# Optimization experiments

Hardware: AMD Instinct MI355X
Metric: run time of the kernel (lower is better)

The kernel has to match this reference:

```python
import jax, jax.numpy as jnp
import numpy as np
import math

N_QUBITS = 8
N_QLAYERS = 1
LN_EPS = 1e-5


def _rx(state, theta, wire, n):
    # state: (N, 2,...,2) complex64 with n qubit axes; theta: (N,)
    sh = (theta.shape[0],) + (1,) * (n - 1)
    c = jnp.cos(theta / 2).reshape(sh)
    s = jnp.sin(theta / 2).reshape(sh)
    a = jax.lax.index_in_dim(state, 0, wire + 1, keepdims=False)
    b = jax.lax.index_in_dim(state, 1, wire + 1, keepdims=False)
    return jnp.stack([c * a - 1j * s * b, -1j * s * a + c * b], axis=wire + 1)


def _cnot(state, cw, tw, n):
    s0 = jax.lax.index_in_dim(state, 0, cw + 1, keepdims=False)
    s1 = jax.lax.index_in_dim(state, 1, cw + 1, keepdims=False)
    t_ax = tw + 1 if tw < cw else tw  # target axis index after removing control axis
    s1 = jnp.flip(s1, axis=t_ax)
    return jnp.stack([s0, s1], axis=cw + 1)


def _quantum(angles, qweights):
    # AngleEmbedding (RX) + BasicEntanglerLayers (RX + CNOT ring) + PauliZ expvals
    # angles: (N, 8) float; qweights: (1, 8) float -> returns (N, 8) float
    n = N_QUBITS
    N = angles.shape[0]
    state = jnp.zeros((N,) + (2,) * n, jnp.complex64)
    state = state.at[(slice(None),) + (0,) * n].set(1.0 + 0j)
    for w in range(n):
        state = _rx(state, angles[:, w], w, n)
    for l in range(N_QLAYERS):
        for w in range(n):
            state = _rx(state, jnp.broadcast_to(qweights[l, w], (N,)), w, n)
        for cw in range(n):
            state = _cnot(state, cw, (cw + 1) % n, n)
    probs = state.real ** 2 + state.imag ** 2
    zs = []
    for w in range(n):
        p = probs.sum(axis=tuple(a for a in range(1, n + 1) if a != w + 1))  # (N, 2)
        zs.append(p[:, 0] - p[:, 1])
    return jnp.stack(zs, axis=-1)


def _layernorm(x, g, b):
    m = x.mean(-1, keepdims=True)
    v = ((x - m) ** 2).mean(-1, keepdims=True)
    return (x - m) / jnp.sqrt(v + LN_EPS) * g + b


def _forward(x, Wq, Wk, Wv, Wo, ln1_g, ln1_b, W1, b1, W2, b2, ln2_g, ln2_b,
             ql1_w, ql1_b, qweights, ql2_w, ql2_b):
    B, S, D = x.shape
    H = 16
    dk = D // H
    q = (x @ Wq.T).reshape(B, S, H, dk)
    k = (x @ Wk.T).reshape(B, S, H, dk)
    v = (x @ Wv.T).reshape(B, S, H, dk)
    scores = jnp.einsum('bqhd,bkhd->bhqk', q, k) * (1.0 / math.sqrt(dk))
    attn = jax.nn.softmax(scores, axis=-1)
    o = jnp.einsum('bhqk,bkhd->bqhd', attn, v).reshape(B, S, D) @ Wo.T
    x = _layernorm(o + x, ln1_g, ln1_b)
    ff = jax.nn.relu(x @ W1.T + b1) @ W2.T + b2
    x = _layernorm(ff + x, ln2_g, ln2_b)
    angles = (x @ ql1_w.T + ql1_b).reshape(B * S, N_QUBITS)
    z = _quantum(angles, qweights).reshape(B, S, N_QUBITS).astype(x.dtype)
    y = jnp.concatenate([z, x], axis=2) @ ql2_w.T + ql2_b
    return y


def setup_inputs() -> dict:
    key = jax.random.key(0)
    ks = jax.random.split(key, 12)
    B, S, D, F = 4, 1024, 1024, 4096
    sc = 0.02
    w = lambda k, *sh: jax.random.normal(k, sh, jnp.float32) * sc
    return {
        'x': jax.random.normal(ks[0], (B, S, D), jnp.float32),
        'Wq': w(ks[1], D, D), 'Wk': w(ks[2], D, D), 'Wv': w(ks[3], D, D), 'Wo': w(ks[4], D, D),
        'ln1_g': jnp.ones((D,), jnp.float32), 'ln1_b': jnp.zeros((D,), jnp.float32),
        'W1': w(ks[5], F, D), 'b1': jnp.zeros((F,), jnp.float32),
        'W2': w(ks[6], D, F), 'b2': jnp.zeros((D,), jnp.float32),
        'ln2_g': jnp.ones((D,), jnp.float32), 'ln2_b': jnp.zeros((D,), jnp.float32),
        'ql1_w': w(ks[7], N_QUBITS, D), 'ql1_b': jnp.zeros((N_QUBITS,), jnp.float32),
        'qweights': jax.random.uniform(ks[8], (N_QLAYERS, N_QUBITS), jnp.float32, 0.0, 2 * np.pi),
        'ql2_w': w(ks[9], D, D + N_QUBITS), 'ql2_b': jnp.zeros((D,), jnp.float32),
    }


def reference(x, Wq, Wk, Wv, Wo, ln1_g, ln1_b, W1, b1, W2, b2, ln2_g, ln2_b,
              ql1_w, ql1_b, qweights, ql2_w, ql2_b):
    return _forward(x, Wq, Wk, Wv, Wo, ln1_g, ln1_b, W1, b1, W2, b2, ln2_g, ln2_b,
                    ql1_w, ql1_b, qweights, ql2_w, ql2_b)
```

## Files before the change

### kernel.cpp

```cpp
#include <hip/hip_runtime.h>
#include <hip/hip_bf16.h>

typedef __bf16 bf16_t;
typedef __attribute__((ext_vector_type(8))) __bf16 bf16x8;
typedef __attribute__((ext_vector_type(4))) float floatx4;

#define BM 128

enum { EPI_NONE = 0, EPI_RESID, EPI_BIAS_RELU, EPI_BIAS_RESID, EPI_QL2 };

__device__ __forceinline__ void gld_lds16(const bf16_t* g, bf16_t* l) {
  __builtin_amdgcn_global_load_lds(
      (__attribute__((address_space(1))) void*)(g),
      (__attribute__((address_space(3))) void*)(l), 16, 0, 0);
}

template<int ROWS, int COLS>
__device__ __forceinline__ void stage_swz(const bf16_t* g, int ld, bf16_t* lds, int tid) {
  constexpr int G = COLS / 8;
  #pragma unroll
  for (int i = 0; i < ROWS * G / 256; ++i) {
    int ci = i * 256 + tid;
    int row = ci / G, cc = ci % G;
    int gg = (G == 8) ? (cc ^ (row & 7)) : ((cc & 8) | ((cc & 7) ^ (row & 7)));
    gld_lds16(g + (size_t)row * ld + gg * 8, lds + ci * 8);
  }
}

__device__ __forceinline__ void core128(const bf16_t* __restrict__ Ag,
                                        const bf16_t* __restrict__ Bg,
                                        int K, int ldb,
                                        bf16_t* As, bf16_t* Bs,
                                        floatx4 acc[4][4]) {
  const int tid = threadIdx.x;
  const int wid = tid >> 6, lane = tid & 63;
  const int wm = (wid >> 1) * 64, wn = (wid & 1) * 64;
  const int m16 = lane & 15, quad = lane >> 4;
  const int r7 = m16 & 7;
  for (int k0 = 0; k0 < K; k0 += 64) {
    stage_swz<128, 64>(Ag + k0, K, As, tid);
    stage_swz<128, 64>(Bg + k0, ldb, Bs, tid);
    __syncthreads();
    #pragma unroll
    for (int ks = 0; ks < 2; ++ks) {
      const int gi = ks * 4 + quad;
      const int slot = gi ^ r7;
      bf16x8 af[4], bfr[4];
      #pragma unroll
      for (int mt = 0; mt < 4; ++mt)
        af[mt] = *(const bf16x8*)&As[((wm + mt * 16 + m16) * 8 + slot) * 8];
      #pragma unroll
      for (int nt = 0; nt < 4; ++nt)
        bfr[nt] = *(const bf16x8*)&Bs[((wn + nt * 16 + m16) * 8 + slot) * 8];
      #pragma unroll
      for (int mt = 0; mt < 4; ++mt)
        #pragma unroll
        for (int nt = 0; nt < 4; ++nt)
          acc[mt][nt] = __builtin_amdgcn_mfma_f32_16x16x32_bf16(af[mt], bfr[nt], acc[mt][nt], 0, 0, 0);
    }
    __syncthreads();
  }
}

template<int EPI>
__global__ __launch_bounds__(256)
void gemm128(const bf16_t* __restrict__ A, const bf16_t* __restrict__ B,
             bf16_t* __restrict__ C, const float* __restrict__ bias,
             int N, int K) {
  __shared__ bf16_t As[BM * 64];
  __shared__ bf16_t Bs[BM * 64];
  const int tid = threadIdx.x;
  const int wid = tid >> 6, lane = tid & 63;
  const int wm = (wid >> 1) * 64, wn = (wid & 1) * 64;
  const int m16 = lane & 15, quad = lane >> 4;
  const int m0 = blockIdx.y * BM, n0 = blockIdx.x * BM;
  floatx4 acc[4][4];
  const floatx4 vzero = {0.f, 0.f, 0.f, 0.f};
  #pragma unroll
  for (int mt = 0; mt < 4; ++mt)
    #pragma unroll
    for (int nt = 0; nt < 4; ++nt) acc[mt][nt] = vzero;
  core128(A + (size_t)m0 * K, B + (size_t)n0 * K, K, K, As, Bs, acc);
  #pragma unroll
  for (int mt = 0; mt < 4; ++mt)
    #pragma unroll
    for (int nt = 0; nt < 4; ++nt) {
      const int gcol = n0 + wn + nt * 16 + m16;
      float bv = (EPI == EPI_BIAS_RELU) ? bias[gcol] : 0.f;
      #pragma unroll
      for (int r = 0; r < 4; ++r) {
        const int grow = m0 + wm + mt * 16 + quad * 4 + r;
        float v = acc[mt][nt][r];
        if (EPI == EPI_BIAS_RELU) { v += bv; v = fmaxf(v, 0.f); }
        C[(size_t)grow * N + gcol] = (bf16_t)v;
      }
    }
}

__global__ __launch_bounds__(256)
void gemm_qkv(const bf16_t* __restrict__ X, const bf16_t* __restrict__ Wb,
              bf16_t* __restrict__ Qo, bf16_t* __restrict__ Ko, bf16_t* __restrict__ Vt) {
  __shared__ bf16_t As[BM * 64];
  __shared__ bf16_t Bs[BM * 64];
  const int tid = threadIdx.x;
  const int wid = tid >> 6, lane = tid & 63;
  const int wm = (wid >> 1) * 64, wn = (wid & 1) * 64;
  const int m16 = lane & 15, quad = lane >> 4;
  const int m0 = blockIdx.y * BM, n0 = blockIdx.x * BM;
  const int sel = blockIdx.z;
  const bf16_t* B = Wb + (size_t)sel * 1024 * 1024;
  floatx4 acc[4][4];
  const floatx4 vzero = {0.f, 0.f, 0.f, 0.f};
  #pragma unroll
  for (int mt = 0; mt < 4; ++mt)
    #pragma unroll
    for (int nt = 0; nt < 4; ++nt) acc[mt][nt] = vzero;
  core128(X + (size_t)m0 * 1024, B + (size_t)n0 * 1024, 1024, 1024, As, Bs, acc);
  if (sel < 2) {
    bf16_t* C = sel ? Ko : Qo;
    const float sc = sel ? 1.f : 0.125f;
    #pragma unroll
    for (int mt = 0; mt < 4; ++mt)
      #pragma unroll
      for (int nt = 0; nt < 4; ++nt) {
        const int gcol = n0 + wn + nt * 16 + m16;
        #pragma unroll
        for (int r = 0; r < 4; ++r) {
          const int grow = m0 + wm + mt * 16 + quad * 4 + r;
          C[(size_t)grow * 1024 + gcol] = (bf16_t)(acc[mt][nt][r] * sc);
        }
      }
  } else {
    #pragma unroll
    for (int mt = 0; mt < 4; ++mt) {
      const int grow0 = m0 + wm + mt * 16 + quad * 4;
      const int b = grow0 >> 10, s = grow0 & 1023;
      #pragma unroll
      for (int nt = 0; nt < 4; ++nt) {
        const int gcol = n0 + wn + nt * 16 + m16;
        const int h = gcol >> 6, d = gcol & 63;
        #pragma unroll
        for (int r = 0; r < 4; ++r)
          Vt[(((size_t)b * 16 + h) * 64 + d) * 1024 + s + r] = (bf16_t)acc[mt][nt][r];
      }
    }
  }
}

template<int EPI, bool OUTF32>
__global__ __launch_bounds__(256)
void gemm64(const bf16_t* __restrict__ A, const bf16_t* __restrict__ B,
            void* __restrict__ Cv,
            const bf16_t* __restrict__ resid, const float* __restrict__ bias,
            const bf16_t* __restrict__ z, const float* __restrict__ zw,
            int N, int K, int ldb, int boff, int mblocks) {
  __shared__ bf16_t As[BM * 128];
  __shared__ bf16_t Bs[64 * 128];
  const int tid = threadIdx.x;
  const int wid = tid >> 6, lane = tid & 63;
  const int wm = (wid >> 1) * 64, wn = (wid & 1) * 32;
  const int m16 = lane & 15, quad = lane >> 4;
  const int r7 = m16 & 7;
  const int id = blockIdx.x;
  const int m0 = (id % mblocks) * BM, n0 = (id / mblocks) * 64;
  const bf16_t* Ag = A + (size_t)m0 * K;
  const bf16_t* Bg = B + (size_t)n0 * ldb + boff;
  floatx4 acc[4][2];
  const floatx4 vzero = {0.f, 0.f, 0.f, 0.f};
  #pragma unroll
  for (int mt = 0; mt < 4; ++mt)
    #pragma unroll
    for (int nt = 0; nt < 2; ++nt) acc[mt][nt] = vzero;
  for (int k0 = 0; k0 < K; k0 += 128) {
    stage_swz<128, 128>(Ag + k0, K, As, tid);
    stage_swz<64, 128>(Bg + k0, ldb, Bs, tid);
    __syncthreads();
    #pragma unroll
    for (int ks = 0; ks < 4; ++ks) {
      const int gi = ks * 4 + quad;
      const int slot = (gi & 8) | ((gi & 7) ^ r7);
      bf16x8 af[4], bfr[2];
      #pragma unroll
      for (int mt = 0; mt < 4; ++mt)
        af[mt] = *(const bf16x8*)&As[((wm + mt * 16 + m16) * 16 + slot) * 8];
      #pragma unroll
      for (int nt = 0; nt < 2; ++nt)
        bfr[nt] = *(const bf16x8*)&Bs[((wn + nt * 16 + m16) * 16 + slot) * 8];
      #pragma unroll
      for (int mt = 0; mt < 4; ++mt)
        #pragma unroll
        for (int nt = 0; nt < 2; ++nt)
          acc[mt][nt] = __builtin_amdgcn_mfma_f32_16x16x32_bf16(af[mt], bfr[nt], acc[mt][nt], 0, 0, 0);
    }
    __syncthreads();
  }
  #pragma unroll
  for (int mt = 0; mt < 4; ++mt)
    #pragma unroll
    for (int nt = 0; nt < 2; ++nt) {
      const int gcol = n0 + wn + nt * 16 + m16;
      float bv = 0.f;
      if (EPI == EPI_BIAS_RESID || EPI == EPI_QL2) bv = bias[gcol];
      #pragma unroll
      for (int r = 0; r < 4; ++r) {
        const int grow = m0 + wm + mt * 16 + quad * 4 + r;
        float v = acc[mt][nt][r];
        if (EPI == EPI_RESID) v += (float)resid[(size_t)grow * N + gcol];
        if (EPI == EPI_BIAS_RESID) v += bv + (float)resid[(size_t)grow * N + gcol];
        if (EPI == EPI_QL2) {
          float s = 0.f;
          #pragma unroll
          for (int u = 0; u < 8; ++u)
            s += (float)z[(size_t)grow * 8 + u] * zw[(size_t)gcol * 1032 + u];
          v += bv + s;
        }
        if (OUTF32) ((float*)Cv)[(size_t)grow * N + gcol] = v;
        else        ((bf16_t*)Cv)[(size_t)grow * N + gcol] = (bf16_t)v;
      }
    }
}

__global__ __launch_bounds__(256)
void attn_kernel(const bf16_t* __restrict__ Q, const bf16_t* __restrict__ Kb,
                 const bf16_t* __restrict__ Vt, bf16_t* __restrict__ O) {
  __shared__ bf16_t Qs[64 * 64];
  __shared__ bf16_t Ks[128 * 64];
  __shared__ bf16_t Vs[64 * 128];
  __shared__ bf16_t Ps[4][16 * 128];
  const int tid = threadIdx.x;
  const int wid = tid >> 6, lane = tid & 63;
  const int m16 = lane & 15, quad = lane >> 4;
  const int qt = blockIdx.x, bh = blockIdx.y;
  const int b = bh >> 4, h = bh & 15;
  const size_t qbase = ((size_t)(b * 1024 + qt * 64)) * 1024 + h * 64;
  #pragma unroll
  for (int i = 0; i < 2; ++i) {
    int ci = i * 256 + tid;
    int row = ci >> 3, cc = ci & 7;
    *(bf16x8*)&Qs[row * 64 + ((cc ^ (row & 7)) * 8)] =
        *(const bf16x8*)&Q[qbase + (size_t)row * 1024 + cc * 8];
  }
  __syncthreads();
  const int qm = wid * 16 + m16;
  bf16x8 qf0 = *(const bf16x8*)&Qs[qm * 64 + ((quad ^ (qm & 7)) * 8)];
  bf16x8 qf1 = *(const bf16x8*)&Qs[qm * 64 + (((4 + quad) ^ (qm & 7)) * 8)];
  floatx4 oacc[4];
  float rs[4];
  const floatx4 vzero = {0.f, 0.f, 0.f, 0.f};
  #pragma unroll
  for (int dt = 0; dt < 4; ++dt) oacc[dt] = vzero;
  #pragma unroll
  for (int r = 0; r < 4; ++r) rs[r] = 0.f;
  const size_t kbase = ((size_t)(b * 1024)) * 1024 + h * 64;
  const size_t vbase = ((size_t)bh * 64) * 1024;
  for (int kt = 0; kt < 8; ++kt) {
    __syncthreads();
    #pragma unroll
    for (int i = 0; i < 4; ++i) {
      int ci = i * 256 + tid;
      int row = ci >> 3, cc = ci & 7;
      *(bf16x8*)&Ks[row * 64 + ((cc ^ (row & 7)) * 8)] =
          *(const bf16x8*)&Kb[kbase + (size_t)(kt * 128 + row) * 1024 + cc * 8];
    }
    #pragma unroll
    for (int i = 0; i < 4; ++i) {
      int ci = i * 256 + tid;
      int dr = ci >> 4, cc = ci & 15;
      int gs = (cc & 8) | ((cc & 7) ^ (dr & 7));
      *(bf16x8*)&Vs[dr * 128 + gs * 8] =
          *(const bf16x8*)&Vt[vbase + (size_t)dr * 1024 + kt * 128 + cc * 8];
    }
    __syncthreads();
    floatx4 sa[8];
    #pragma unroll
    for (int nt = 0; nt < 8; ++nt) sa[nt] = vzero;
    #pragma unroll
    for (int nt = 0; nt < 8; ++nt) {
      const int n = nt * 16 + m16;
      bf16x8 kf0 = *(const bf16x8*)&Ks[n * 64 + ((quad ^ (n & 7)) * 8)];
      bf16x8 kf1 = *(const bf16x8*)&Ks[n * 64 + (((4 + quad) ^ (n & 7)) * 8)];
      sa[nt] = __builtin_amdgcn_mfma_f32_16x16x32_bf16(qf0, kf0, sa[nt], 0, 0, 0);
      sa[nt] = __builtin_amdgcn_mfma_f32_16x16x32_bf16(qf1, kf1, sa[nt], 0, 0, 0);
    }
    #pragma unroll
    for (int nt = 0; nt < 8; ++nt)
      #pragma unroll
      for (int r = 0; r < 4; ++r) {
        float pv = __expf(sa[nt][r]);
        rs[r] += pv;
        const int prow = quad * 4 + r;
        const int g = nt * 2 + (m16 >> 3);
        const int gs = (g & 8) | ((g & 7) ^ (prow & 7));
        Ps[wid][prow * 128 + gs * 8 + (m16 & 7)] = (bf16_t)pv;
      }
    bf16x8 pf[4];
    #pragma unroll
    for (int ksub = 0; ksub < 4; ++ksub) {
      const int g = ksub * 4 + quad;
      const int gs = (g & 8) | ((g & 7) ^ (m16 & 7));
      pf[ksub] = *(const bf16x8*)&Ps[wid][m16 * 128 + gs * 8];
    }
    #pragma unroll
    for (int dt = 0; dt < 4; ++dt) {
      const int n = dt * 16 + m16;
      #pragma unroll
      for (int ksub = 0; ksub < 4; ++ksub) {
        const int g = ksub * 4 + quad;
        const int gs = (g & 8) | ((g & 7) ^ (n & 7));
        bf16x8 vf = *(const bf16x8*)&Vs[n * 128 + gs * 8];
        oacc[dt] = __builtin_amdgcn_mfma_f32_16x16x32_bf16(pf[ksub], vf, oacc[dt], 0, 0, 0);
      }
    }
  }
  #pragma unroll
  for (int r = 0; r < 4; ++r) {
    rs[r] += __shfl_xor(rs[r], 1);
    rs[r] += __shfl_xor(rs[r], 2);
    rs[r] += __shfl_xor(rs[r], 4);
    rs[r] += __shfl_xor(rs[r], 8);
  }
  const size_t obase = ((size_t)(b * 1024 + qt * 64 + wid * 16)) * 1024 + h * 64;
  #pragma unroll
  for (int dt = 0; dt < 4; ++dt)
    #pragma unroll
    for (int r = 0; r < 4; ++r)
      O[obase + (size_t)(quad * 4 + r) * 1024 + dt * 16 + m16] = (bf16_t)(oacc[dt][r] / rs[r]);
}

struct Segs {
  const float* s[5];
  bf16_t* d[5];
  int n8[5];
};
__global__ __launch_bounds__(256)
void conv_multi(Segs sg) {
  const int zz = blockIdx.z;
  const float* in = sg.s[zz];
  bf16_t* out = sg.d[zz];
  const int n8 = sg.n8[zz];
  for (int i = blockIdx.x * 256 + threadIdx.x; i < n8; i += gridDim.x * 256) {
    const float* p = in + (size_t)i * 8;
    floatx4 a = *(const floatx4*)p;
    floatx4 b = *(const floatx4*)(p + 4);
    bf16x8 o;
    #pragma unroll
    for (int j = 0; j < 4; ++j) { o[j] = (bf16_t)a[j]; o[4 + j] = (bf16_t)b[j]; }
    *(bf16x8*)(out + (size_t)i * 8) = o;
  }
}

__global__ __launch_bounds__(256)
void ln_kernel(const bf16_t* __restrict__ in, const float* __restrict__ g,
               const float* __restrict__ b, bf16_t* __restrict__ out) {
  const int row = blockIdx.x * 4 + (threadIdx.x >> 6);
  const int lane = threadIdx.x & 63;
  const bf16_t* p = in + (size_t)row * 1024 + lane * 16;
  bf16x8 v0 = *(const bf16x8*)p;
  bf16x8 v1 = *(const bf16x8*)(p + 8);
  float f[16];
  #pragma unroll
  for (int j = 0; j < 8; ++j) { f[j] = (float)v0[j]; f[8 + j] = (float)v1[j]; }
  float s = 0.f, ss = 0.f;
  #pragma unroll
  for (int j = 0; j < 16; ++j) { s += f[j]; ss += f[j] * f[j]; }
  #pragma unroll
  for (int off = 1; off < 64; off <<= 1) { s += __shfl_xor(s, off); ss += __shfl_xor(ss, off); }
  const float m = s * (1.f / 1024.f);
  const float inv_sd = rsqrtf(ss * (1.f / 1024.f) - m * m + 1e-5f);
  const float* gp = g + lane * 16;
  const float* bp = b + lane * 16;
  bf16x8 o0, o1;
  #pragma unroll
  for (int j = 0; j < 8; ++j) o0[j] = (bf16_t)((f[j] - m) * inv_sd * gp[j] + bp[j]);
  #pragma unroll
  for (int j = 0; j < 8; ++j) o1[j] = (bf16_t)((f[8 + j] - m) * inv_sd * gp[8 + j] + bp[8 + j]);
  *(bf16x8*)&out[(size_t)row * 1024 + lane * 16] = o0;
  *(bf16x8*)&out[(size_t)row * 1024 + lane * 16 + 8] = o1;
}

__global__ __launch_bounds__(256)
void ln2_quantum(const bf16_t* __restrict__ in, const float* __restrict__ g,
                 const float* __restrict__ b, bf16_t* __restrict__ x2,
                 const float* __restrict__ qw1, const float* __restrict__ qb1,
                 const float* __restrict__ qwt, bf16_t* __restrict__ zout,
                 const float* __restrict__ ql2w, bf16_t* __restrict__ ql2wb) {
  if (blockIdx.z == 1) {
    const int n8 = 1024 * 1032 / 8;
    for (int i = blockIdx.x * 256 + threadIdx.x; i < n8; i += gridDim.x * 256) {
      const float* p = ql2w + (size_t)i * 8;
      floatx4 a = *(const floatx4*)p;
      floatx4 bb = *(const floatx4*)(p + 4);
      bf16x8 o;
      #pragma unroll
      for (int j = 0; j < 4; ++j) { o[j] = (bf16_t)a[j]; o[4 + j] = (bf16_t)bb[j]; }
      *(bf16x8*)(ql2wb + (size_t)i * 8) = o;
    }
    return;
  }
  const int row = blockIdx.x * 4 + (threadIdx.x >> 6);
  const int lane = threadIdx.x & 63;
  const bf16_t* p = in + (size_t)row * 1024 + lane * 16;
  bf16x8 v0 = *(const bf16x8*)p;
  bf16x8 v1 = *(const bf16x8*)(p + 8);
  float f[16];
  #pragma unroll
  for (int j = 0; j < 8; ++j) { f[j] = (float)v0[j]; f[8 + j] = (float)v1[j]; }
  float s = 0.f, ss = 0.f;
  #pragma unroll
  for (int j = 0; j < 16; ++j) { s += f[j]; ss += f[j] * f[j]; }
  #pragma unroll
  for (int off = 1; off < 64; off <<= 1) { s += __shfl_xor(s, off); ss += __shfl_xor(ss, off); }
  const float m = s * (1.f / 1024.f);
  const float inv_sd = rsqrtf(ss * (1.f / 1024.f) - m * m + 1e-5f);
  const float* gp = g + lane * 16;
  const float* bp = b + lane * 16;
  bf16x8 o0, o1;
  #pragma unroll
  for (int j = 0; j < 8; ++j) o0[j] = (bf16_t)((f[j] - m) * inv_sd * gp[j] + bp[j]);
  #pragma unroll
  for (int j = 0; j < 8; ++j) o1[j] = (bf16_t)((f[8 + j] - m) * inv_sd * gp[8 + j] + bp[8 + j]);
  *(bf16x8*)&x2[(size_t)row * 1024 + lane * 16] = o0;
  *(bf16x8*)&x2[(size_t)row * 1024 + lane * 16 + 8] = o1;
  float th[8];
  #pragma unroll
  for (int qq = 0; qq < 8; ++qq) {
    const float* wp = qw1 + (size_t)qq * 1024 + lane * 16;
    float sdot = 0.f;
    #pragma unroll
    for (int j = 0; j < 8; ++j)
      sdot += (float)o0[j] * wp[j] + (float)o1[j] * wp[8 + j];
    #pragma unroll
    for (int off = 1; off < 64; off <<= 1) sdot += __shfl_xor(sdot, off);
    th[qq] = sdot + qb1[qq] + qwt[qq];
  }
  if (lane == 0) {
    float c[8];
    #pragma unroll
    for (int qq = 0; qq < 8; ++qq) c[qq] = cosf(th[qq]);
    float z0 = 1.f;
    #pragma unroll
    for (int u = 1; u < 8; ++u) z0 *= c[u];
    zout[(size_t)row * 8 + 0] = (bf16_t)z0;
    float pp = c[0];
    #pragma unroll
    for (int w = 1; w < 8; ++w) { pp *= c[w]; zout[(size_t)row * 8 + w] = (bf16_t)pp; }
  }
}

extern "C" void kernel_launch(void* const* d_in, const int* in_sizes, int n_in,
                              void* d_out, int out_size, void* d_ws, size_t ws_size,
                              hipStream_t stream) {
  const float* x    = (const float*)d_in[0];
  const float* Wq   = (const float*)d_in[1];
  const float* Wk   = (const float*)d_in[2];
  const float* Wv   = (const float*)d_in[3];
  const float* Wo   = (const float*)d_in[4];
  const float* ln1g = (const float*)d_in[5];
  const float* ln1b = (const float*)d_in[6];
  const float* W1   = (const float*)d_in[7];
  const float* b1   = (const float*)d_in[8];
  const float* W2   = (const float*)d_in[9];
  const float* b2   = (const float*)d_in[10];
  const float* ln2g = (const float*)d_in[11];
  const float* ln2b = (const float*)d_in[12];
  const float* qw1  = (const float*)d_in[13];
  const float* qb1  = (const float*)d_in[14];
  const float* qwt  = (const float*)d_in[15];
  const float* ql2w = (const float*)d_in[16];
  const float* ql2b = (const float*)d_in[17];
  bf16_t* ws = (bf16_t*)d_ws;

  const size_t T = (size_t)4096 * 1024;
  const size_t M1 = (size_t)1024 * 1024;
  bf16_t* outlo = (bf16_t*)d_out;
  bf16_t* outhi = outlo + T;

  bf16_t* xb    = ws;
  bf16_t* kb    = ws + T;
  bf16_t* vt    = ws + 2 * T;
  bf16_t* ff    = ws + 3 * T;
  bf16_t* wqkvb = ff;
  bf16_t* wob   = ff + 3 * M1;
  bf16_t* w1b   = vt;
  bf16_t* w2b   = kb;
  bf16_t* ql2wb = vt;
  bf16_t* q     = outlo;
  bf16_t* o     = outhi;
  bf16_t* x1p   = outlo;
  bf16_t* x1    = outhi;
  bf16_t* x2p   = outlo;
  bf16_t* x2    = xb;
  bf16_t* z     = kb;

  {
    Segs sg;
    sg.s[0] = x;  sg.d[0] = xb;            sg.n8[0] = (int)(T / 8);
    sg.s[1] = Wq; sg.d[1] = wqkvb;         sg.n8[1] = (int)(M1 / 8);
    sg.s[2] = Wk; sg.d[2] = wqkvb + M1;    sg.n8[2] = (int)(M1 / 8);
    sg.s[3] = Wv; sg.d[3] = wqkvb + 2*M1;  sg.n8[3] = (int)(M1 / 8);
    sg.s[4] = Wo; sg.d[4] = wob;           sg.n8[4] = (int)(M1 / 8);
    conv_multi<<<dim3(512, 1, 5), 256, 0, stream>>>(sg);
  }
  gemm_qkv<<<dim3(8, 32, 3), 256, 0, stream>>>(xb, wqkvb, q, kb, vt);
  attn_kernel<<<dim3(16, 64), 256, 0, stream>>>(q, kb, vt, o);
  gemm64<EPI_RESID, false><<<512, 256, 0, stream>>>(
      o, wob, x1p, xb, nullptr, nullptr, nullptr, 1024, 1024, 1024, 0, 32);
  ln_kernel<<<1024, 256, 0, stream>>>(x1p, ln1g, ln1b, x1);
  {
    Segs sg;
    sg.s[0] = W1; sg.d[0] = w1b; sg.n8[0] = (int)(T / 8);
    sg.s[1] = W2; sg.d[1] = w2b; sg.n8[1] = (int)(T / 8);
    sg.s[2] = nullptr; sg.d[2] = nullptr; sg.n8[2] = 0;
    sg.s[3] = nullptr; sg.d[3] = nullptr; sg.n8[3] = 0;
    sg.s[4] = nullptr; sg.d[4] = nullptr; sg.n8[4] = 0;
    conv_multi<<<dim3(1024, 1, 2), 256, 0, stream>>>(sg);
  }
  gemm128<EPI_BIAS_RELU><<<dim3(32, 32), 256, 0, stream>>>(x1, w1b, ff, b1, 4096, 1024);
  gemm64<EPI_BIAS_RESID, false><<<512, 256, 0, stream>>>(
      ff, w2b, x2p, x1, b2, nullptr, nullptr, 1024, 4096, 4096, 0, 32);
  ln2_quantum<<<dim3(1024, 1, 2), 256, 0, stream>>>(
      x2p, ln2g, ln2b, x2, qw1, qb1, qwt, z, ql2w, ql2wb);
  gemm64<EPI_QL2, true><<<512, 256, 0, stream>>>(
      x2, ql2wb, d_out, nullptr, ql2b, z, ql2w, 1024, 1024, 1032, 8, 32);
}
```

Measured before the change: 400.6 us.

## Split-K the Wo and W2 GEMMs into two partials combined in layernorm

The Wo and W2 projection GEMMs now run with a 2-way K split, doubling the grid from 512 to 1024 blocks. Each half writes a bf16 partial to a separate buffer. The layernorm kernels sum the two partials plus the residual (and bias for LN2) before normalising. The aim is better CU occupancy on the 512-block launches, at the cost of extra partial-buffer traffic, an extra bf16 rounding of partials, and reshuffled workspace aliasing.

```diff
diff --git a/kernel.cpp b/kernel.cpp
--- a/kernel.cpp
+++ b/kernel.cpp
@@ -7,7 +7,7 @@
 
 #define BM 128
 
-enum { EPI_NONE = 0, EPI_RESID, EPI_BIAS_RELU, EPI_BIAS_RESID, EPI_QL2 };
+enum { EPI_NONE = 0, EPI_RESID, EPI_BIAS_RELU, EPI_BIAS_RESID, EPI_QL2, EPI_PART };
 
 __device__ __forceinline__ void gld_lds16(const bf16_t* g, bf16_t* l) {
   __builtin_amdgcn_global_load_lds(
@@ -150,10 +150,10 @@
 template<int EPI, bool OUTF32>
 __global__ __launch_bounds__(256)
 void gemm64(const bf16_t* __restrict__ A, const bf16_t* __restrict__ B,
-            void* __restrict__ Cv,
+            void* __restrict__ Cv, bf16_t* __restrict__ part1,
             const bf16_t* __restrict__ resid, const float* __restrict__ bias,
             const bf16_t* __restrict__ z, const float* __restrict__ zw,
-            int N, int K, int ldb, int boff, int mblocks) {
+            int N, int K, int ldb, int boff, int mblocks, int nblocks) {
   __shared__ bf16_t As[BM * 128];
   __shared__ bf16_t Bs[64 * 128];
   const int tid = threadIdx.x;
@@ -162,16 +162,21 @@
   const int m16 = lane & 15, quad = lane >> 4;
   const int r7 = m16 & 7;
   const int id = blockIdx.x;
-  const int m0 = (id % mblocks) * BM, n0 = (id / mblocks) * 64;
-  const bf16_t* Ag = A + (size_t)m0 * K;
-  const bf16_t* Bg = B + (size_t)n0 * ldb + boff;
+  const int m0 = (id % mblocks) * BM;
+  const int rest = id / mblocks;
+  const int n0 = (rest % nblocks) * 64;
+  const int kh = rest / nblocks;
+  const int ksplit = gridDim.x / (mblocks * nblocks);
+  const int Keff = K / ksplit;
+  const bf16_t* Ag = A + (size_t)m0 * K + (size_t)kh * Keff;
+  const bf16_t* Bg = B + (size_t)n0 * ldb + boff + (size_t)kh * Keff;
   floatx4 acc[4][2];
   const floatx4 vzero = {0.f, 0.f, 0.f, 0.f};
   #pragma unroll
   for (int mt = 0; mt < 4; ++mt)
     #pragma unroll
     for (int nt = 0; nt < 2; ++nt) acc[mt][nt] = vzero;
-  for (int k0 = 0; k0 < K; k0 += 128) {
+  for (int k0 = 0; k0 < Keff; k0 += 128) {
     stage_swz<128, 128>(Ag + k0, K, As, tid);
     stage_swz<64, 128>(Bg + k0, ldb, Bs, tid);
     __syncthreads();
@@ -194,6 +199,7 @@
     }
     __syncthreads();
   }
+  bf16_t* Cp = (EPI == EPI_PART && kh) ? part1 : (bf16_t*)Cv;
   #pragma unroll
   for (int mt = 0; mt < 4; ++mt)
     #pragma unroll
@@ -215,7 +221,7 @@
           v += bv + s;
         }
         if (OUTF32) ((float*)Cv)[(size_t)grow * N + gcol] = v;
-        else        ((bf16_t*)Cv)[(size_t)grow * N + gcol] = (bf16_t)v;
+        else        Cp[(size_t)grow * N + gcol] = (bf16_t)v;
       }
     }
 }
@@ -350,16 +356,25 @@
 }
 
 __global__ __launch_bounds__(256)
-void ln_kernel(const bf16_t* __restrict__ in, const float* __restrict__ g,
-               const float* __restrict__ b, bf16_t* __restrict__ out) {
+void ln_combine(const bf16_t* __restrict__ p0, const bf16_t* __restrict__ p1,
+                const bf16_t* __restrict__ resid,
+                const float* __restrict__ g, const float* __restrict__ b,
+                bf16_t* __restrict__ out) {
   const int row = blockIdx.x * 4 + (threadIdx.x >> 6);
   const int lane = threadIdx.x & 63;
-  const bf16_t* p = in + (size_t)row * 1024 + lane * 16;
-  bf16x8 v0 = *(const bf16x8*)p;
-  bf16x8 v1 = *(const bf16x8*)(p + 8);
+  const size_t base = (size_t)row * 1024 + lane * 16;
+  bf16x8 a0 = *(const bf16x8*)&p0[base];
+  bf16x8 a1 = *(const bf16x8*)&p0[base + 8];
+  bf16x8 b0 = *(const bf16x8*)&p1[base];
+  bf16x8 b1 = *(const bf16x8*)&p1[base + 8];
+  bf16x8 c0 = *(const bf16x8*)&resid[base];
+  bf16x8 c1 = *(const bf16x8*)&resid[base + 8];
   float f[16];
   #pragma unroll
-  for (int j = 0; j < 8; ++j) { f[j] = (float)v0[j]; f[8 + j] = (float)v1[j]; }
+  for (int j = 0; j < 8; ++j) {
+    f[j]     = (float)a0[j] + (float)b0[j] + (float)c0[j];
+    f[8 + j] = (float)a1[j] + (float)b1[j] + (float)c1[j];
+  }
   float s = 0.f, ss = 0.f;
   #pragma unroll
   for (int j = 0; j < 16; ++j) { s += f[j]; ss += f[j] * f[j]; }
@@ -374,13 +389,15 @@
   for (int j = 0; j < 8; ++j) o0[j] = (bf16_t)((f[j] - m) * inv_sd * gp[j] + bp[j]);
   #pragma unroll
   for (int j = 0; j < 8; ++j) o1[j] = (bf16_t)((f[8 + j] - m) * inv_sd * gp[8 + j] + bp[8 + j]);
-  *(bf16x8*)&out[(size_t)row * 1024 + lane * 16] = o0;
-  *(bf16x8*)&out[(size_t)row * 1024 + lane * 16 + 8] = o1;
-}
-
-__global__ __launch_bounds__(256)
-void ln2_quantum(const bf16_t* __restrict__ in, const float* __restrict__ g,
-                 const float* __restrict__ b, bf16_t* __restrict__ x2,
+  *(bf16x8*)&out[base] = o0;
+  *(bf16x8*)&out[base + 8] = o1;
+}
+
+__global__ __launch_bounds__(256)
+void ln2_quantum(const bf16_t* __restrict__ p0, const bf16_t* __restrict__ p1,
+                 const bf16_t* __restrict__ resid, const float* __restrict__ bias,
+                 const float* __restrict__ g, const float* __restrict__ b,
+                 bf16_t* __restrict__ x2,
                  const float* __restrict__ qw1, const float* __restrict__ qb1,
                  const float* __restrict__ qwt, bf16_t* __restrict__ zout,
                  const float* __restrict__ ql2w, bf16_t* __restrict__ ql2wb) {
@@ -399,12 +416,20 @@
   }
   const int row = blockIdx.x * 4 + (threadIdx.x >> 6);
   const int lane = threadIdx.x & 63;
-  const bf16_t* p = in + (size_t)row * 1024 + lane * 16;
-  bf16x8 v0 = *(const bf16x8*)p;
-  bf16x8 v1 = *(const bf16x8*)(p + 8);
+  const size_t base = (size_t)row * 1024 + lane * 16;
+  bf16x8 a0 = *(const bf16x8*)&p0[base];
+  bf16x8 a1 = *(const bf16x8*)&p0[base + 8];
+  bf16x8 b0 = *(const bf16x8*)&p1[base];
+  bf16x8 b1 = *(const bf16x8*)&p1[base + 8];
+  bf16x8 c0 = *(const bf16x8*)&resid[base];
+  bf16x8 c1 = *(const bf16x8*)&resid[base + 8];
+  const float* bsp = bias + lane * 16;
   float f[16];
   #pragma unroll
-  for (int j = 0; j < 8; ++j) { f[j] = (float)v0[j]; f[8 + j] = (float)v1[j]; }
+  for (int j = 0; j < 8; ++j) {
+    f[j]     = (float)a0[j] + (float)b0[j] + (float)c0[j] + bsp[j];
+    f[8 + j] = (float)a1[j] + (float)b1[j] + (float)c1[j] + bsp[8 + j];
+  }
   float s = 0.f, ss = 0.f;
   #pragma unroll
   for (int j = 0; j < 16; ++j) { s += f[j]; ss += f[j] * f[j]; }
@@ -419,8 +444,8 @@
   for (int j = 0; j < 8; ++j) o0[j] = (bf16_t)((f[j] - m) * inv_sd * gp[j] + bp[j]);
   #pragma unroll
   for (int j = 0; j < 8; ++j) o1[j] = (bf16_t)((f[8 + j] - m) * inv_sd * gp[8 + j] + bp[8 + j]);
-  *(bf16x8*)&x2[(size_t)row * 1024 + lane * 16] = o0;
-  *(bf16x8*)&x2[(size_t)row * 1024 + lane * 16 + 8] = o1;
+  *(bf16x8*)&x2[base] = o0;
+  *(bf16x8*)&x2[base + 8] = o1;
   float th[8];
   #pragma unroll
   for (int qq = 0; qq < 8; ++qq) {
@@ -483,13 +508,11 @@
   bf16_t* wob   = ff + 3 * M1;
   bf16_t* w1b   = vt;
   bf16_t* w2b   = kb;
-  bf16_t* ql2wb = vt;
+  bf16_t* ql2wb = ff;
   bf16_t* q     = outlo;
   bf16_t* o     = outhi;
-  bf16_t* x1p   = outlo;
   bf16_t* x1    = outhi;
-  bf16_t* x2p   = outlo;
-  bf16_t* x2    = xb;
+  bf16_t* x2    = vt;
   bf16_t* z     = kb;
 
   {
@@ -503,9 +526,9 @@
   }
   gemm_qkv<<<dim3(8, 32, 3), 256, 0, stream>>>(xb, wqkvb, q, kb, vt);
   attn_kernel<<<dim3(16, 64), 256, 0, stream>>>(q, kb, vt, o);
-  gemm64<EPI_RESID, false><<<512, 256, 0, stream>>>(
-      o, wob, x1p, xb, nullptr, nullptr, nullptr, 1024, 1024, 1024, 0, 32);
-  ln_kernel<<<1024, 256, 0, stream>>>(x1p, ln1g, ln1b, x1);
+  gemm64<EPI_PART, false><<<1024, 256, 0, stream>>>(
+      o, wob, outlo, kb, nullptr, nullptr, nullptr, nullptr, 1024, 1024, 1024, 0, 32, 16);
+  ln_combine<<<1024, 256, 0, stream>>>(outlo, kb, xb, ln1g, ln1b, x1);
   {
     Segs sg;
     sg.s[0] = W1; sg.d[0] = w1b; sg.n8[0] = (int)(T / 8);
@@ -516,10 +539,10 @@
     conv_multi<<<dim3(1024, 1, 2), 256, 0, stream>>>(sg);
   }
   gemm128<EPI_BIAS_RELU><<<dim3(32, 32), 256, 0, stream>>>(x1, w1b, ff, b1, 4096, 1024);
-  gemm64<EPI_BIAS_RESID, false><<<512, 256, 0, stream>>>(
-      ff, w2b, x2p, x1, b2, nullptr, nullptr, 1024, 4096, 4096, 0, 32);
+  gemm64<EPI_PART, false><<<1024, 256, 0, stream>>>(
+      ff, w2b, xb, vt, nullptr, nullptr, nullptr, nullptr, 1024, 4096, 4096, 0, 32, 16);
   ln2_quantum<<<dim3(1024, 1, 2), 256, 0, stream>>>(
-      x2p, ln2g, ln2b, x2, qw1, qb1, qwt, z, ql2w, ql2wb);
+      xb, vt, x1, b2, ln2g, ln2b, x2, qw1, qb1, qwt, z, ql2w, ql2wb);
   gemm64<EPI_QL2, true><<<512, 256, 0, stream>>>(
-      x2, ql2wb, d_out, nullptr, ql2b, z, ql2w, 1024, 1024, 1032, 8, 32);
-}
+      x2, ql2wb, d_out, nullptr, nullptr, ql2b, z, ql2w, 1024, 1024, 1032, 8, 32, 16);
+}
```

Result: no change. 401.6 us (+0.2%).
